# Kernel tuning notes

Measured on AMD Instinct MI355X. Metric: run time of the kernel, lower is better.

The kernel has to match this reference:

```python
import jax, jax.numpy as jnp
import numpy as np


def log_g(x):
    # log of g(x) = where(x>=0, x+0.5, sigmoid(x))
    return jnp.where(x >= 0, jnp.log(jax.nn.relu(x) + 0.5), -jax.nn.softplus(-x))


def heinsen_scan_log(log_coeffs, log_values):
    # associative scan in log space over seq dim (axis=1)
    a_star = jnp.cumsum(log_coeffs, axis=1)
    log_h0_plus_b_star = jax.lax.cumlogsumexp(log_values - a_star, axis=1)
    return jnp.exp(a_star + log_h0_plus_b_star)


def setup_inputs() -> dict:
    key = jax.random.key(0)
    k1, k2, k3 = jax.random.split(key, 3)
    B, S, D_IN, D_INNER, D_OUT = 4, 4096, 1024, 1024, 1024
    x = jax.random.normal(k1, (B, S, D_IN), dtype=jnp.float32)
    # xavier_normal for Linear(d_in, 2*d_inner): std = sqrt(2/(fan_in+fan_out))
    std_hg = float(np.sqrt(2.0 / (D_IN + 2 * D_INNER)))
    W_hg = jax.random.normal(k2, (2 * D_INNER, D_IN), dtype=jnp.float32) * std_hg
    std_out = float(np.sqrt(2.0 / (D_INNER + D_OUT)))
    W_out = jax.random.normal(k3, (D_OUT, D_INNER), dtype=jnp.float32) * std_out
    return {"x": x, "W_hg": W_hg, "W_out": W_out}


def reference(x, W_hg, W_out):
    # x: [B,S,Din]; W_hg: [2*Dinner, Din]; W_out: [Dout, Dinner]
    hg = jnp.einsum("bsd,ed->bse", x, W_hg)
    hidden, gate = jnp.split(hg, 2, axis=-1)
    log_coeffs = -jax.nn.softplus(gate)        # log(1 - z)
    log_z = -jax.nn.softplus(-gate)            # log(z)
    log_values = log_z + log_g(hidden)
    h = heinsen_scan_log(log_coeffs, log_values)  # [B,S,Dinner]
    out = jnp.einsum("bsd,od->bso", h, W_out)
    return out
```

## Files before the change

kernel.cpp:

```cpp
#include <hip/hip_runtime.h>
#include <math.h>


typedef unsigned short ushort_t;
typedef __attribute__((ext_vector_type(4))) float f32x4;
typedef __attribute__((ext_vector_type(8))) __bf16 bf16x8;
typedef __attribute__((ext_vector_type(8))) unsigned short u16x8;

constexpr int Bsz  = 4;
constexpr int S    = 4096;
constexpr int Din  = 1024;
constexpr int Dh   = 1024;
constexpr int M    = Bsz * S;
constexpr int NCH  = 64;
constexpr int CL   = S / NCH;

__device__ __forceinline__ unsigned short f2bf(float f) {
    unsigned int u = __float_as_uint(f);
    unsigned int r = (u + 0x7fffu + ((u >> 16) & 1u)) >> 16;
    return (unsigned short)r;
}
__device__ __forceinline__ float bf2f(unsigned short u) {
    return __uint_as_float(((unsigned int)u) << 16);
}
__device__ __forceinline__ float sigf(float x) {
    x = fminf(fmaxf(x, -30.f), 30.f);
    return 1.0f / (1.0f + __expf(-x));
}
__device__ __forceinline__ void gld_lds16(const ushort_t* g, ushort_t* l) {
    __builtin_amdgcn_global_load_lds(
        (const __attribute__((address_space(1))) void*)g,
        (__attribute__((address_space(3))) void*)l, 16, 0, 0);
}

__global__ __launch_bounds__(256) void cvt_bf16(
    const float* __restrict__ in, ushort_t* __restrict__ out, int n8)
{
    const int i = blockIdx.x * 256 + threadIdx.x;
    if (i >= n8) return;
    const float4 a = ((const float4*)in)[i * 2];
    const float4 b = ((const float4*)in)[i * 2 + 1];
    u16x8 o;
    o[0] = f2bf(a.x); o[1] = f2bf(a.y); o[2] = f2bf(a.z); o[3] = f2bf(a.w);
    o[4] = f2bf(b.x); o[5] = f2bf(b.y); o[6] = f2bf(b.z); o[7] = f2bf(b.w);
    ((u16x8*)out)[i] = o;
}

template<bool OUT_BF16>
__global__ __launch_bounds__(512, 2) void gemm256(
    const ushort_t* __restrict__ A, int lda,
    const ushort_t* __restrict__ B, int ldb,
    void* __restrict__ Cout, int ldc, int K, int nbx_log2)
{
    __shared__ ushort_t lds[4][2][8192];

    const int P = K >> 5;

    const int nwg = gridDim.x;
    const int cpx = nwg >> 3;
    const int b   = blockIdx.x;
    const int swz = (b & 7) * cpx + (b >> 3);
    const int bx  = swz & ((1 << nbx_log2) - 1);
    const int by  = swz >> nbx_log2;
    const int bm0 = by * 256;
    const int bn0 = bx * 256;

    const int t  = threadIdx.x;
    const int w  = t >> 6;
    const int l  = t & 63;
    const int wr = w >> 2;
    const int wc = w & 3;

    const int fr = l & 15;
    const int kg = l >> 4;
    const int qp = kg ^ (((fr >> 3) & 1) << 1);
    const int a_base = wr * 4096 + fr * 32 + qp * 8;
    const int b_base = wc * 2048 + fr * 32 + qp * 8;

    const int rs = l >> 2;
    const int lq = (l & 3) ^ (((rs >> 3) & 1) << 1);
    const ushort_t* gA0 = A + (size_t)(bm0 + w * 16 + rs) * lda + lq * 8;
    const ushort_t* gA1 = gA0 + (size_t)128 * lda;
    const ushort_t* gB0 = B + (size_t)(bn0 + w * 16 + rs) * ldb + lq * 8;
    const ushort_t* gB1 = gB0 + (size_t)128 * ldb;

    f32x4 acc[8][4];
    #pragma unroll
    for (int i = 0; i < 8; ++i)
        #pragma unroll
        for (int j = 0; j < 4; ++j)
            acc[i][j] = (f32x4){0.f, 0.f, 0.f, 0.f};

    auto stage = [&](int p) {
        const int s2 = p & 3;
        const int ko = p * 32;
        gld_lds16(gA0 + ko, &lds[s2][0][w * 512]);
        gld_lds16(gA1 + ko, &lds[s2][0][w * 512 + 4096]);
        gld_lds16(gB0 + ko, &lds[s2][1][w * 512]);
        gld_lds16(gB1 + ko, &lds[s2][1][w * 512 + 4096]);
    };

    auto phase_body = [&](int p, bool do_stage) {
        __builtin_amdgcn_s_barrier();
        __builtin_amdgcn_sched_barrier(0);
        const int s = p & 3;
        const ushort_t* la = &lds[s][0][0];
        const ushort_t* lb = &lds[s][1][0];
        bf16x8 af[8], bfr[4];
        #pragma unroll
        for (int i = 0; i < 8; ++i)
            af[i] = *(const bf16x8*)&la[a_base + i * 512];
        #pragma unroll
        for (int j = 0; j < 4; ++j)
            bfr[j] = *(const bf16x8*)&lb[b_base + j * 512];
        if (do_stage) stage(p + 2);
        __builtin_amdgcn_sched_barrier(0);
        __builtin_amdgcn_s_setprio(1);
        #pragma unroll
        for (int i = 0; i < 8; ++i)
            #pragma unroll
            for (int j = 0; j < 4; ++j)
                acc[i][j] = __builtin_amdgcn_mfma_f32_16x16x32_bf16(
                    af[i], bfr[j], acc[i][j], 0, 0, 0);
        __builtin_amdgcn_s_setprio(0);
        __builtin_amdgcn_sched_barrier(0);
    };

    stage(0);
    stage(1);

    for (int p = 0; p < P - 1; ++p) {
        asm volatile("s_waitcnt vmcnt(4)" ::: "memory");
        phase_body(p, p < P - 2);
    }
    asm volatile("s_waitcnt vmcnt(0)" ::: "memory");
    phase_body(P - 1, false);

    #pragma unroll
    for (int i = 0; i < 8; ++i) {
        #pragma unroll
        for (int j = 0; j < 4; ++j) {
            const int col = bn0 + wc * 64 + j * 16 + fr;
            #pragma unroll
            for (int r = 0; r < 4; ++r) {
                const int row = bm0 + wr * 128 + i * 16 + kg * 4 + r;
                if (OUT_BF16)
                    ((ushort_t*)Cout)[(size_t)row * ldc + col] = f2bf(acc[i][j][r]);
                else
                    ((float*)Cout)[(size_t)row * ldc + col] = acc[i][j][r];
            }
        }
    }
}


__global__ __launch_bounds__(256) void scan_stage1(
    const ushort_t* __restrict__ hg, float* __restrict__ Abuf,
    float* __restrict__ hlbuf)
{
    const int g     = blockIdx.x * 256 + threadIdx.x;
    const int d     = g & (Dh - 1);
    const int chunk = (g >> 10) & (NCH - 1);
    const int b     = g >> 16;
    const size_t rowbase = (size_t)(b * S + chunk * CL) * 2048;
    float h = 0.0f, Aacc = 1.0f;
    #pragma unroll 4
    for (int i = 0; i < CL; ++i) {
        const float hid  = bf2f(hg[rowbase + (size_t)i * 2048 + d]);
        const float gate = bf2f(hg[rowbase + (size_t)i * 2048 + 1024 + d]);
        const float z  = sigf(gate);
        const float c  = sigf(-gate);
        const float gv = (hid >= 0.0f) ? (hid + 0.5f) : sigf(hid);
        h = fmaf(c, h, z * gv);
        Aacc *= c;
    }
    const size_t o = (size_t)(b * NCH + chunk) * Dh + d;
    Abuf[o]  = Aacc;
    hlbuf[o] = h;
}

__global__ __launch_bounds__(256) void scan_stage2(
    const float* __restrict__ Abuf, const float* __restrict__ hlbuf,
    float* __restrict__ Hs)
{
    const int g = blockIdx.x * 256 + threadIdx.x;
    const int d = g & (Dh - 1);
    const int b = g >> 10;
    float h = 0.0f;
    for (int ch = 0; ch < NCH; ++ch) {
        const size_t o = (size_t)(b * NCH + ch) * Dh + d;
        Hs[o] = h;
        h = fmaf(Abuf[o], h, hlbuf[o]);
    }
}

__global__ __launch_bounds__(256) void scan_stage3(
    const ushort_t* __restrict__ hg, const float* __restrict__ Hs,
    ushort_t* __restrict__ hout)
{
    const int g     = blockIdx.x * 256 + threadIdx.x;
    const int d     = g & (Dh - 1);
    const int chunk = (g >> 10) & (NCH - 1);
    const int b     = g >> 16;
    const size_t rowbase = (size_t)(b * S + chunk * CL) * 2048;
    const size_t hbase   = (size_t)(b * S + chunk * CL) * 1024 + d;
    float h = Hs[(size_t)(b * NCH + chunk) * Dh + d];
    #pragma unroll 4
    for (int i = 0; i < CL; ++i) {
        const size_t ro = rowbase + (size_t)i * 2048;
        const float hid  = bf2f(hg[ro + d]);
        const float gate = bf2f(hg[ro + 1024 + d]);
        const float z  = sigf(gate);
        const float c  = sigf(-gate);
        const float gv = (hid >= 0.0f) ? (hid + 0.5f) : sigf(hid);
        h = fmaf(c, h, z * gv);
        hout[hbase + (size_t)i * 1024] = f2bf(h);
    }
}

extern "C" void kernel_launch(void* const* d_in, const int* in_sizes, int n_in,
                              void* d_out, int out_size, void* d_ws, size_t ws_size,
                              hipStream_t stream)
{
    (void)in_sizes; (void)n_in; (void)out_size; (void)ws_size;
    const float* x    = (const float*)d_in[0];
    const float* Whg  = (const float*)d_in[1];
    const float* Wout = (const float*)d_in[2];
    float* out = (float*)d_out;

    ushort_t* hgbuf = (ushort_t*)d_ws;
    ushort_t* xb    = hgbuf + (size_t)M * 2048;
    ushort_t* whgb  = xb + (size_t)M * 1024;
    ushort_t* woutb = whgb + (size_t)2048 * 1024;
    float*    Abuf  = (float*)(woutb + (size_t)1024 * 1024);
    float*    hlbuf = Abuf + (size_t)Bsz * NCH * Dh;
    float*    Hsbuf = hlbuf + (size_t)Bsz * NCH * Dh;

    const dim3 blk(256);

    cvt_bf16<<<dim3(M * Din / 8 / 256), blk, 0, stream>>>(x, xb, M * Din / 8);
    cvt_bf16<<<dim3(2048 * 1024 / 8 / 256), blk, 0, stream>>>(Whg, whgb, 2048 * 1024 / 8);
    cvt_bf16<<<dim3(1024 * 1024 / 8 / 256), blk, 0, stream>>>(Wout, woutb, 1024 * 1024 / 8);

    gemm256<true><<<dim3(512), dim3(512), 0, stream>>>(
        xb, Din, whgb, Din, hgbuf, 2048, Din, 3);

    scan_stage1<<<dim3(Bsz * NCH * Dh / 256), blk, 0, stream>>>(hgbuf, Abuf, hlbuf);
    scan_stage2<<<dim3(Bsz * Dh / 256), blk, 0, stream>>>(Abuf, hlbuf, Hsbuf);
    scan_stage3<<<dim3(Bsz * NCH * Dh / 256), blk, 0, stream>>>(hgbuf, Hsbuf, xb);

    gemm256<false><<<dim3(256), dim3(512), 0, stream>>>(
        xb, Dh, woutb, Din, out, 1024, Dh, 2);
}
```

Baseline: 215.5 us.

## Restructure GEMM into K=64 double-buffered tiles with quarter-step staging; fuse conversions

The GEMM main loop now uses 64-wide K tiles in a double buffer instead of four 32-wide stages. Each tile is split into four sub-phases that reuse B fragments across the two M halves, and loads for later tiles are interleaved between MFMA blocks with a new XOR swizzle on the LDS layout. The aim is to cut LDS fragment reloads and barrier stalls and to overlap global loads with compute more finely. The three fp32-to-bf16 conversion launches are merged into one kernel to save launch overhead. The risks are the more intricate vmcnt bookkeeping and possible new LDS bank conflicts from the swizzle.

Result: no change. 211.6 us (-1.8%).

```diff
diff --git a/kernel.cpp b/kernel.cpp
--- a/kernel.cpp
+++ b/kernel.cpp
@@ -33,17 +33,25 @@
         (__attribute__((address_space(3))) void*)l, 16, 0, 0);
 }
 
-__global__ __launch_bounds__(256) void cvt_bf16(
-    const float* __restrict__ in, ushort_t* __restrict__ out, int n8)
-{
+__global__ __launch_bounds__(256) void cvt_all(
+    const float* __restrict__ x, const float* __restrict__ whg,
+    const float* __restrict__ wout,
+    ushort_t* __restrict__ xb, ushort_t* __restrict__ whgb,
+    ushort_t* __restrict__ woutb)
+{
+    constexpr int NX = M * Din / 8;
+    constexpr int NW = 2048 * 1024 / 8;
     const int i = blockIdx.x * 256 + threadIdx.x;
-    if (i >= n8) return;
-    const float4 a = ((const float4*)in)[i * 2];
-    const float4 b = ((const float4*)in)[i * 2 + 1];
+    const float* src; ushort_t* dst; int k;
+    if (i < NX)            { src = x;    dst = xb;    k = i; }
+    else if (i < NX + NW)  { src = whg;  dst = whgb;  k = i - NX; }
+    else                   { src = wout; dst = woutb; k = i - NX - NW; }
+    const float4 a = ((const float4*)src)[(size_t)k * 2];
+    const float4 b = ((const float4*)src)[(size_t)k * 2 + 1];
     u16x8 o;
     o[0] = f2bf(a.x); o[1] = f2bf(a.y); o[2] = f2bf(a.z); o[3] = f2bf(a.w);
     o[4] = f2bf(b.x); o[5] = f2bf(b.y); o[6] = f2bf(b.z); o[7] = f2bf(b.w);
-    ((u16x8*)out)[i] = o;
+    ((u16x8*)dst)[k] = o;
 }
 
 template<bool OUT_BF16>
@@ -52,14 +60,15 @@
     const ushort_t* __restrict__ B, int ldb,
     void* __restrict__ Cout, int ldc, int K, int nbx_log2)
 {
-    __shared__ ushort_t lds[4][2][8192];
-
-    const int P = K >> 5;
+    __shared__ ushort_t lds[2][2][16384];
+    char* const ldsb = (char*)&lds[0][0][0];
+
+    const int NT = K >> 6;
 
     const int nwg = gridDim.x;
     const int cpx = nwg >> 3;
-    const int b   = blockIdx.x;
-    const int swz = (b & 7) * cpx + (b >> 3);
+    const int bid = blockIdx.x;
+    const int swz = (bid & 7) * cpx + (bid >> 3);
     const int bx  = swz & ((1 << nbx_log2) - 1);
     const int by  = swz >> nbx_log2;
     const int bm0 = by * 256;
@@ -73,16 +82,36 @@
 
     const int fr = l & 15;
     const int kg = l >> 4;
-    const int qp = kg ^ (((fr >> 3) & 1) << 1);
-    const int a_base = wr * 4096 + fr * 32 + qp * 8;
-    const int b_base = wc * 2048 + fr * 32 + qp * 8;
-
-    const int rs = l >> 2;
-    const int lq = (l & 3) ^ (((rs >> 3) & 1) << 1);
-    const ushort_t* gA0 = A + (size_t)(bm0 + w * 16 + rs) * lda + lq * 8;
-    const ushort_t* gA1 = gA0 + (size_t)128 * lda;
-    const ushort_t* gB0 = B + (size_t)(bn0 + w * 16 + rs) * ldb + lq * 8;
-    const ushort_t* gB1 = gB0 + (size_t)128 * ldb;
+    const int a_row_byte = fr * 128;
+    const int a_col0 = (kg * 16) ^ ((fr & 7) << 4);
+    const int a_col1 = a_col0 ^ 64;
+    const int b_row_byte = (wc * 64 + fr) * 64
+                         + ((kg * 16) ^ (((fr >> 1) & 3) << 4));
+
+    const int rA      = w * 16 + (l >> 3);
+    const int rowA0p  = ((rA     ) >> 6) * 128 + ((rA     ) & 63);
+    const int rowA1p  = ((rA +  8) >> 6) * 128 + ((rA +  8) & 63);
+    const int acolA   = (((l & 7) * 16) ^ (((l >> 3) & 7) << 4)) >> 1;
+    const ushort_t* aS0 = A + (size_t)(bm0 + rowA0p) * lda + acolA;
+    const ushort_t* aS1 = A + (size_t)(bm0 + rowA1p) * lda + acolA;
+    const size_t aMh = (size_t)64 * lda;
+    const int brA  = w * 32 + (l >> 2);
+    const int bcol = ((l & 3) ^ ((l >> 3) & 3)) * 8;
+    const ushort_t* bS0 = B + (size_t)(bn0 + brA) * ldb + bcol;
+    const ushort_t* bS1 = bS0 + (size_t)16 * ldb;
+
+    auto stageA = [&](int Tt, int mh) {
+        char* db = ldsb + (size_t)(Tt & 1) * 65536 + mh * 16384 + w * 2048;
+        const size_t go = (size_t)mh * aMh + Tt * 64;
+        gld_lds16(aS0 + go, (ushort_t*)db);
+        gld_lds16(aS1 + go, (ushort_t*)(db + 1024));
+    };
+    auto stageB = [&](int Tt, int ks) {
+        char* db = ldsb + (size_t)(Tt & 1) * 65536 + 32768 + ks * 16384 + w * 2048;
+        const int go = Tt * 64 + ks * 32;
+        gld_lds16(bS0 + go, (ushort_t*)db);
+        gld_lds16(bS1 + go, (ushort_t*)(db + 1024));
+    };
 
     f32x4 acc[8][4];
     #pragma unroll
@@ -91,50 +120,109 @@
         for (int j = 0; j < 4; ++j)
             acc[i][j] = (f32x4){0.f, 0.f, 0.f, 0.f};
 
-    auto stage = [&](int p) {
-        const int s2 = p & 3;
-        const int ko = p * 32;
-        gld_lds16(gA0 + ko, &lds[s2][0][w * 512]);
-        gld_lds16(gA1 + ko, &lds[s2][0][w * 512 + 4096]);
-        gld_lds16(gB0 + ko, &lds[s2][1][w * 512]);
-        gld_lds16(gB1 + ko, &lds[s2][1][w * 512 + 4096]);
-    };
-
-    auto phase_body = [&](int p, bool do_stage) {
+    bf16x8 bfr0[4], bfr1[4];
+
+    stageB(0, 0); stageB(0, 1); stageA(0, 0); stageA(0, 1);
+    stageB(1, 0); stageB(1, 1); stageA(1, 0);
+    asm volatile("s_waitcnt vmcnt(6)" ::: "memory");
+
+    #pragma unroll 1
+    for (int T = 0; T < NT; ++T) {
+        if (T == NT - 1)
+            asm volatile("s_waitcnt vmcnt(0)" ::: "memory");
+        const char* abuf = ldsb + (size_t)(T & 1) * 65536;
+        const char* bbuf = abuf + 32768;
+
         __builtin_amdgcn_s_barrier();
         __builtin_amdgcn_sched_barrier(0);
-        const int s = p & 3;
-        const ushort_t* la = &lds[s][0][0];
-        const ushort_t* lb = &lds[s][1][0];
-        bf16x8 af[8], bfr[4];
-        #pragma unroll
-        for (int i = 0; i < 8; ++i)
-            af[i] = *(const bf16x8*)&la[a_base + i * 512];
-        #pragma unroll
-        for (int j = 0; j < 4; ++j)
-            bfr[j] = *(const bf16x8*)&lb[b_base + j * 512];
-        if (do_stage) stage(p + 2);
-        __builtin_amdgcn_sched_barrier(0);
-        __builtin_amdgcn_s_setprio(1);
-        #pragma unroll
-        for (int i = 0; i < 8; ++i)
+        if (T + 1 < NT) stageA(T + 1, 1);
+        asm volatile("s_waitcnt vmcnt(8)" ::: "memory");
+        __builtin_amdgcn_sched_barrier(0);
+        {
             #pragma unroll
             for (int j = 0; j < 4; ++j)
-                acc[i][j] = __builtin_amdgcn_mfma_f32_16x16x32_bf16(
-                    af[i], bfr[j], acc[i][j], 0, 0, 0);
-        __builtin_amdgcn_s_setprio(0);
-        __builtin_amdgcn_sched_barrier(0);
-    };
-
-    stage(0);
-    stage(1);
-
-    for (int p = 0; p < P - 1; ++p) {
-        asm volatile("s_waitcnt vmcnt(4)" ::: "memory");
-        phase_body(p, p < P - 2);
-    }
-    asm volatile("s_waitcnt vmcnt(0)" ::: "memory");
-    phase_body(P - 1, false);
+                bfr0[j] = *(const bf16x8*)(bbuf + j * 1024 + b_row_byte);
+            bf16x8 af[4];
+            #pragma unroll
+            for (int i = 0; i < 4; ++i)
+                af[i] = *(const bf16x8*)(abuf + wr * 8192 + i * 2048 + a_row_byte + a_col0);
+            __builtin_amdgcn_s_setprio(1);
+            #pragma unroll
+            for (int i = 0; i < 4; ++i)
+                #pragma unroll
+                for (int j = 0; j < 4; ++j)
+                    acc[i][j] = __builtin_amdgcn_mfma_f32_16x16x32_bf16(
+                        af[i], bfr0[j], acc[i][j], 0, 0, 0);
+            __builtin_amdgcn_s_setprio(0);
+            __builtin_amdgcn_sched_barrier(0);
+        }
+
+        __builtin_amdgcn_s_barrier();
+        __builtin_amdgcn_sched_barrier(0);
+        if (T + 2 < NT) stageB(T + 2, 0);
+        asm volatile("s_waitcnt vmcnt(8)" ::: "memory");
+        __builtin_amdgcn_sched_barrier(0);
+        {
+            #pragma unroll
+            for (int j = 0; j < 4; ++j)
+                bfr1[j] = *(const bf16x8*)(bbuf + 16384 + j * 1024 + b_row_byte);
+            bf16x8 af[4];
+            #pragma unroll
+            for (int i = 0; i < 4; ++i)
+                af[i] = *(const bf16x8*)(abuf + wr * 8192 + i * 2048 + a_row_byte + a_col1);
+            __builtin_amdgcn_s_setprio(1);
+            #pragma unroll
+            for (int i = 0; i < 4; ++i)
+                #pragma unroll
+                for (int j = 0; j < 4; ++j)
+                    acc[i][j] = __builtin_amdgcn_mfma_f32_16x16x32_bf16(
+                        af[i], bfr1[j], acc[i][j], 0, 0, 0);
+            __builtin_amdgcn_s_setprio(0);
+            __builtin_amdgcn_sched_barrier(0);
+        }
+
+        __builtin_amdgcn_s_barrier();
+        __builtin_amdgcn_sched_barrier(0);
+        if (T + 2 < NT) stageB(T + 2, 1);
+        asm volatile("s_waitcnt vmcnt(8)" ::: "memory");
+        __builtin_amdgcn_sched_barrier(0);
+        {
+            bf16x8 af[4];
+            #pragma unroll
+            for (int i = 0; i < 4; ++i)
+                af[i] = *(const bf16x8*)(abuf + 16384 + wr * 8192 + i * 2048 + a_row_byte + a_col0);
+            __builtin_amdgcn_s_setprio(1);
+            #pragma unroll
+            for (int i = 0; i < 4; ++i)
+                #pragma unroll
+                for (int j = 0; j < 4; ++j)
+                    acc[4 + i][j] = __builtin_amdgcn_mfma_f32_16x16x32_bf16(
+                        af[i], bfr0[j], acc[4 + i][j], 0, 0, 0);
+            __builtin_amdgcn_s_setprio(0);
+            __builtin_amdgcn_sched_barrier(0);
+        }
+
+        __builtin_amdgcn_s_barrier();
+        __builtin_amdgcn_sched_barrier(0);
+        if (T + 2 < NT) stageA(T + 2, 0);
+        asm volatile("s_waitcnt vmcnt(8)" ::: "memory");
+        __builtin_amdgcn_sched_barrier(0);
+        {
+            bf16x8 af[4];
+            #pragma unroll
+            for (int i = 0; i < 4; ++i)
+                af[i] = *(const bf16x8*)(abuf + 16384 + wr * 8192 + i * 2048 + a_row_byte + a_col1);
+            __builtin_amdgcn_s_setprio(1);
+            #pragma unroll
+            for (int i = 0; i < 4; ++i)
+                #pragma unroll
+                for (int j = 0; j < 4; ++j)
+                    acc[4 + i][j] = __builtin_amdgcn_mfma_f32_16x16x32_bf16(
+                        af[i], bfr1[j], acc[4 + i][j], 0, 0, 0);
+            __builtin_amdgcn_s_setprio(0);
+            __builtin_amdgcn_sched_barrier(0);
+        }
+    }
 
     #pragma unroll
     for (int i = 0; i < 8; ++i) {
@@ -238,9 +326,7 @@
 
     const dim3 blk(256);
 
-    cvt_bf16<<<dim3(M * Din / 8 / 256), blk, 0, stream>>>(x, xb, M * Din / 8);
-    cvt_bf16<<<dim3(2048 * 1024 / 8 / 256), blk, 0, stream>>>(Whg, whgb, 2048 * 1024 / 8);
-    cvt_bf16<<<dim3(1024 * 1024 / 8 / 256), blk, 0, stream>>>(Wout, woutb, 1024 * 1024 / 8);
+    cvt_all<<<dim3(9728), blk, 0, stream>>>(x, Whg, Wout, xb, whgb, woutb);
 
     gemm256<true><<<dim3(512), dim3(512), 0, stream>>>(
         xb, Din, whgb, Din, hgbuf, 2048, Din, 3);
```

## Stage GEMM epilogue through LDS for vector stores, restructure pipeline, merge conversions

Applied to the files above, without the earlier changes.

The GEMM epilogue now writes each wave's accumulator tile into LDS and reads it back row-contiguous. This turns scattered scalar global stores into 16-byte (fp32) or 8-byte (bf16) vector stores. The main loop is rewritten as a single non-unrolled loop with explicit barriers and waitcnts placed around the MFMA block, and the three fp32-to-bf16 conversion launches are merged into one kernel. The changes aim to cut store transactions and launch overhead, at the cost of extra LDS round trips and barrier placement that has to remain correct.

Result: slower. 300.1 us (+39.3%).

```diff
diff --git a/kernel.cpp b/kernel.cpp
--- a/kernel.cpp
+++ b/kernel.cpp
@@ -6,6 +6,7 @@
 typedef __attribute__((ext_vector_type(4))) float f32x4;
 typedef __attribute__((ext_vector_type(8))) __bf16 bf16x8;
 typedef __attribute__((ext_vector_type(8))) unsigned short u16x8;
+typedef __attribute__((ext_vector_type(4))) unsigned short u16x4;
 
 constexpr int Bsz  = 4;
 constexpr int S    = 4096;
@@ -33,17 +34,25 @@
         (__attribute__((address_space(3))) void*)l, 16, 0, 0);
 }
 
-__global__ __launch_bounds__(256) void cvt_bf16(
-    const float* __restrict__ in, ushort_t* __restrict__ out, int n8)
-{
+__global__ __launch_bounds__(256) void cvt_all(
+    const float* __restrict__ x, const float* __restrict__ whg,
+    const float* __restrict__ wout,
+    ushort_t* __restrict__ xb, ushort_t* __restrict__ whgb,
+    ushort_t* __restrict__ woutb)
+{
+    constexpr int NX = M * Din / 8;
+    constexpr int NW = 2048 * 1024 / 8;
     const int i = blockIdx.x * 256 + threadIdx.x;
-    if (i >= n8) return;
-    const float4 a = ((const float4*)in)[i * 2];
-    const float4 b = ((const float4*)in)[i * 2 + 1];
+    const float* src; ushort_t* dst; int k;
+    if (i < NX)            { src = x;    dst = xb;    k = i; }
+    else if (i < NX + NW)  { src = whg;  dst = whgb;  k = i - NX; }
+    else                   { src = wout; dst = woutb; k = i - NX - NW; }
+    const float4 a = ((const float4*)src)[(size_t)k * 2];
+    const float4 b = ((const float4*)src)[(size_t)k * 2 + 1];
     u16x8 o;
     o[0] = f2bf(a.x); o[1] = f2bf(a.y); o[2] = f2bf(a.z); o[3] = f2bf(a.w);
     o[4] = f2bf(b.x); o[5] = f2bf(b.y); o[6] = f2bf(b.z); o[7] = f2bf(b.w);
-    ((u16x8*)out)[i] = o;
+    ((u16x8*)dst)[k] = o;
 }
 
 template<bool OUT_BF16>
@@ -53,13 +62,14 @@
     void* __restrict__ Cout, int ldc, int K, int nbx_log2)
 {
     __shared__ ushort_t lds[4][2][8192];
+    char* const ldsb = (char*)&lds[0][0][0];
 
     const int P = K >> 5;
 
     const int nwg = gridDim.x;
     const int cpx = nwg >> 3;
-    const int b   = blockIdx.x;
-    const int swz = (b & 7) * cpx + (b >> 3);
+    const int bid = blockIdx.x;
+    const int swz = (bid & 7) * cpx + (bid >> 3);
     const int bx  = swz & ((1 << nbx_log2) - 1);
     const int by  = swz >> nbx_log2;
     const int bm0 = by * 256;
@@ -100,20 +110,28 @@
         gld_lds16(gB1 + ko, &lds[s2][1][w * 512 + 4096]);
     };
 
-    auto phase_body = [&](int p, bool do_stage) {
-        __builtin_amdgcn_s_barrier();
-        __builtin_amdgcn_sched_barrier(0);
+    stage(0);
+    stage(1);
+    asm volatile("s_waitcnt vmcnt(4)" ::: "memory");
+    __builtin_amdgcn_s_barrier();
+    __builtin_amdgcn_sched_barrier(0);
+
+    #pragma unroll 1
+    for (int p = 0; p < P; ++p) {
         const int s = p & 3;
         const ushort_t* la = &lds[s][0][0];
         const ushort_t* lb = &lds[s][1][0];
         bf16x8 af[8], bfr[4];
         #pragma unroll
         for (int i = 0; i < 8; ++i)
-            af[i] = *(const bf16x8*)&la[a_base + i * 512];
+            af[i] = *reinterpret_cast<const bf16x8*>(&la[a_base + i * 512]);
         #pragma unroll
         for (int j = 0; j < 4; ++j)
-            bfr[j] = *(const bf16x8*)&lb[b_base + j * 512];
-        if (do_stage) stage(p + 2);
+            bfr[j] = *reinterpret_cast<const bf16x8*>(&lb[b_base + j * 512]);
+        if (p + 2 < P) stage(p + 2);
+        __builtin_amdgcn_sched_barrier(0);
+        __builtin_amdgcn_s_barrier();
+        asm volatile("s_waitcnt lgkmcnt(0)" ::: "memory");
         __builtin_amdgcn_sched_barrier(0);
         __builtin_amdgcn_s_setprio(1);
         #pragma unroll
@@ -124,32 +142,41 @@
                     af[i], bfr[j], acc[i][j], 0, 0, 0);
         __builtin_amdgcn_s_setprio(0);
         __builtin_amdgcn_sched_barrier(0);
-    };
-
-    stage(0);
-    stage(1);
-
-    for (int p = 0; p < P - 1; ++p) {
-        asm volatile("s_waitcnt vmcnt(4)" ::: "memory");
-        phase_body(p, p < P - 2);
-    }
-    asm volatile("s_waitcnt vmcnt(0)" ::: "memory");
-    phase_body(P - 1, false);
-
-    #pragma unroll
+        if (p <= P - 3)
+            asm volatile("s_waitcnt vmcnt(4)" ::: "memory");
+        else if (p == P - 2)
+            asm volatile("s_waitcnt vmcnt(0)" ::: "memory");
+        __builtin_amdgcn_s_barrier();
+    }
+
+    float* lw = (float*)(ldsb + w * 4352);
+    #pragma unroll 1
     for (int i = 0; i < 8; ++i) {
-        #pragma unroll
-        for (int j = 0; j < 4; ++j) {
-            const int col = bn0 + wc * 64 + j * 16 + fr;
+        asm volatile("s_waitcnt lgkmcnt(0)" ::: "memory");
+        __builtin_amdgcn_sched_barrier(0);
+        #pragma unroll
+        for (int j = 0; j < 4; ++j)
             #pragma unroll
-            for (int r = 0; r < 4; ++r) {
-                const int row = bm0 + wr * 128 + i * 16 + kg * 4 + r;
-                if (OUT_BF16)
-                    ((ushort_t*)Cout)[(size_t)row * ldc + col] = f2bf(acc[i][j][r]);
-                else
-                    ((float*)Cout)[(size_t)row * ldc + col] = acc[i][j][r];
+            for (int r = 0; r < 4; ++r)
+                lw[(kg * 4 + r) * 68 + j * 16 + fr] = acc[i][j][r];
+        asm volatile("s_waitcnt lgkmcnt(0)" ::: "memory");
+        __builtin_amdgcn_sched_barrier(0);
+        #pragma unroll
+        for (int ci = 0; ci < 4; ++ci) {
+            const int rr  = ci * 4 + kg;
+            const f32x4 v = *(const f32x4*)&lw[rr * 68 + fr * 4];
+            const int row = bm0 + wr * 128 + i * 16 + rr;
+            const int col = bn0 + wc * 64 + fr * 4;
+            if (OUT_BF16) {
+                u16x4 o4;
+                o4[0] = f2bf(v[0]); o4[1] = f2bf(v[1]);
+                o4[2] = f2bf(v[2]); o4[3] = f2bf(v[3]);
+                *(u16x4*)((ushort_t*)Cout + (size_t)row * ldc + col) = o4;
+            } else {
+                *(f32x4*)((float*)Cout + (size_t)row * ldc + col) = v;
             }
         }
+        __builtin_amdgcn_sched_barrier(0);
     }
 }
 
@@ -238,9 +265,7 @@
 
     const dim3 blk(256);
 
-    cvt_bf16<<<dim3(M * Din / 8 / 256), blk, 0, stream>>>(x, xb, M * Din / 8);
-    cvt_bf16<<<dim3(2048 * 1024 / 8 / 256), blk, 0, stream>>>(Whg, whgb, 2048 * 1024 / 8);
-    cvt_bf16<<<dim3(1024 * 1024 / 8 / 256), blk, 0, stream>>>(Wout, woutb, 1024 * 1024 / 8);
+    cvt_all<<<dim3(9728), blk, 0, stream>>>(x, Whg, Wout, xb, whgb, woutb);
 
     gemm256<true><<<dim3(512), dim3(512), 0, stream>>>(
         xb, Din, whgb, Din, hgbuf, 2048, Din, 3);
```
